# Kernel tuning notes

Measured on AMD Instinct MI355X. Metric: run time of the kernel, lower is better.

## Reference

```python
import jax, jax.numpy as jnp
import numpy as np

T_ITERS = 10
EPS = 1e-5


def setup_inputs() -> dict:
    key = jax.random.key(0)
    B, C, H, W = 64, 256, 56, 56
    X = jax.random.normal(key, (B, C, H, W), dtype=jnp.float32)
    # running_rot buffer: orthogonal rotation per group (g=1)
    M = np.random.default_rng(0).standard_normal((C, C)).astype(np.float32)
    q, _ = np.linalg.qr(M)
    running_rot = jnp.asarray(q[None, :, :])  # [g=1, d, d]
    return {"X": X, "running_rot": running_rot}


def _whiten(X, g, nc):
    # X: [B, C, H, W] -> x: [g, d, m] with m = B*H*W (training-mode IterNorm)
    B, C, H, W = X.shape
    x = jnp.transpose(X, (1, 0, 2, 3)).reshape(g, nc, -1)
    m = x.shape[-1]
    mean = jnp.mean(x, axis=-1, keepdims=True)          # [g, d, 1]
    xc = x - mean                                        # [g, d, m]
    I = jnp.broadcast_to(jnp.eye(nc, dtype=X.dtype), (g, nc, nc))
    Sigma = EPS * I + jnp.matmul(xc, jnp.swapaxes(xc, 1, 2)) * (1.0 / m)
    # rTr = 1 / trace(Sigma) per group
    rTr = 1.0 / jnp.sum(Sigma * I, axis=(1, 2), keepdims=True)  # [g,1,1]
    Sigma_N = Sigma * rTr
    # Newton-Schulz iteration: P_{k+1} = 1.5 P_k - 0.5 P_k^3 Sigma_N
    P = I
    for _ in range(T_ITERS):
        P3 = jnp.matmul(jnp.matmul(P, P), P)
        P = 1.5 * P - 0.5 * jnp.matmul(P3, Sigma_N)
    wm = P * jnp.sqrt(rTr)                               # whitening matrix [g,d,d]
    xn = jnp.matmul(wm, xc)                              # [g, d, m]
    return xn.reshape(C, B, H, W).transpose(1, 0, 2, 3)  # back to [B,C,H,W]


def reference(X, running_rot):
    g, _, nc = running_rot.shape
    B, C, H, W = X.shape
    X_hat = _whiten(X, g, nc)                            # [B, C, H, W]
    Xg = X_hat.reshape(B, g, nc, H, W)
    # rotate whitened features: Q^T alignment, einsum('bgchw,gdc->bgdhw')
    Xr = jnp.einsum('bgchw,gdc->bgdhw', Xg, running_rot)
    return Xr.reshape(B, C, H, W)
```

## Files before the change

kernel.cpp:

```cpp
#include <hip/hip_runtime.h>
#include <math.h>

#define HWn   3136
#define Cn    256
#define KCPB  49
#define NCHUNK 3136
#define INV_M (1.0f/200704.0f)
#define EPSc  1e-5f

typedef __attribute__((ext_vector_type(4))) float f32x4;
typedef __attribute__((ext_vector_type(8))) short s16x8;
typedef __attribute__((ext_vector_type(4))) unsigned short u16x4;

static __device__ __forceinline__ unsigned short f2bf(float f) {
  unsigned int u = __builtin_bit_cast(unsigned int, f);
  u = (u + 0x7fffu + ((u >> 16) & 1u)) >> 16;
  return (unsigned short)u;
}

__global__ __launch_bounds__(1024) void k_gram(const float* __restrict__ X,
                                               float* __restrict__ Gp,
                                               float* __restrict__ Sp,
                                               int nparts) {
  __shared__ __align__(16) unsigned short lds[2][256 * 64];
  const int t = threadIdx.x, p = blockIdx.x;
  const int w = t >> 6, l = t & 63, a = l & 15, g = l >> 4;
  const int swzA = (a & 7) << 3;
  const int crow = t >> 4, sg = t & 15;

  f32x4 acc[16];
#pragma unroll
  for (int j = 0; j < 16; ++j) acc[j] = (f32x4){0.f, 0.f, 0.f, 0.f};
  float sum4[4] = {0.f, 0.f, 0.f, 0.f};
  float vx[16];

  const int start = (int)(((long)NCHUNK * p) / nparts);
  const int end   = (int)(((long)NCHUNK * (p + 1)) / nparts);

#define G_LOADS(CH)                                                           \
  {                                                                           \
    const int b_ = (CH) / KCPB, kc_ = (CH) % KCPB;                            \
    const float* xb_ = X + (long)b_ * Cn * HWn + kc_ * 64;                    \
    _Pragma("unroll")                                                         \
    for (int p4 = 0; p4 < 4; ++p4) {                                          \
      const float4 v = *(const float4*)(xb_ + (long)(p4 * 64 + crow) * HWn + sg * 4); \
      vx[p4 * 4 + 0] = v.x; vx[p4 * 4 + 1] = v.y;                             \
      vx[p4 * 4 + 2] = v.z; vx[p4 * 4 + 3] = v.w;                             \
    }                                                                         \
  }

#define G_CVTWR(BUF)                                                          \
  {                                                                           \
    _Pragma("unroll")                                                         \
    for (int p4 = 0; p4 < 4; ++p4) {                                          \
      const int c_ = p4 * 64 + crow;                                          \
      sum4[p4] += (vx[p4 * 4 + 0] + vx[p4 * 4 + 1])                           \
                + (vx[p4 * 4 + 2] + vx[p4 * 4 + 3]);                          \
      u16x4 h;                                                                \
      h.x = f2bf(vx[p4 * 4 + 0]); h.y = f2bf(vx[p4 * 4 + 1]);                 \
      h.z = f2bf(vx[p4 * 4 + 2]); h.w = f2bf(vx[p4 * 4 + 3]);                 \
      *(u16x4*)(&lds[BUF][0] + ((c_ * 64 + sg * 4) ^ ((c_ & 7) << 3))) = h;   \
    }                                                                         \
  }

  G_LOADS(start);
  G_CVTWR(0);
  __syncthreads();

  for (int ch = start; ch < end; ++ch) {
    const int cur = (ch - start) & 1;
    if (ch + 1 < end) G_LOADS(ch + 1);
    const unsigned short* tile = &lds[cur][0];
#pragma unroll
    for (int kk = 0; kk < 64; kk += 32) {
      const s16x8 fw = *(const s16x8*)(tile + (((w * 16 + a) * 64 + kk + g * 8) ^ swzA));
#pragma unroll
      for (int j = 0; j < 16; ++j) {
        const s16x8 fj = *(const s16x8*)(tile + (((j * 16 + a) * 64 + kk + g * 8) ^ swzA));
        acc[j] = __builtin_amdgcn_mfma_f32_16x16x32_bf16(fw, fj, acc[j], 0, 0, 0);
      }
    }
    if (ch + 1 < end) G_CVTWR(cur ^ 1);
    __syncthreads();
  }
#undef G_LOADS
#undef G_CVTWR

  float* gout = Gp + (long)p * 65536;
#pragma unroll
  for (int j = 0; j < 16; ++j)
#pragma unroll
    for (int r = 0; r < 4; ++r)
      gout[(16 * w + 4 * g + r) * 256 + 16 * j + a] = acc[j][r];

#pragma unroll
  for (int p4 = 0; p4 < 4; ++p4) {
    float s = sum4[p4];
    s += __shfl_xor(s, 1);
    s += __shfl_xor(s, 2);
    s += __shfl_xor(s, 4);
    s += __shfl_xor(s, 8);
    if (a == 0) Sp[(long)p * 256 + p4 * 64 + w * 4 + g] = s;
  }
}

__global__ __launch_bounds__(1024) void k_reduce(const float* __restrict__ Gp,
                                                 const float* __restrict__ Sp,
                                                 float* __restrict__ Sigma,
                                                 float* __restrict__ P0,
                                                 float* __restrict__ diag,
                                                 float* __restrict__ meansum,
                                                 int nparts) {
  __shared__ float red[4][256];
  __shared__ float msh[256];
  const int t = threadIdx.x, c = t & 255, g = t >> 8, j = blockIdx.x;
  const long e = (long)j * 256 + c;
  const int p0 = (nparts * g) >> 2, p1 = (nparts * (g + 1)) >> 2;

  {
    float s = 0.f;
    for (int p = p0; p < p1; ++p) s += Sp[(long)p * 256 + c];
    red[g][c] = s;
  }
  __syncthreads();
  if (g == 0) msh[c] = (red[0][c] + red[1][c]) + (red[2][c] + red[3][c]);
  __syncthreads();

  {
    const float* gp = Gp + (long)p0 * 65536 + e;
    const int np = p1 - p0;
    float s0 = 0.f, s1 = 0.f, s2 = 0.f, s3 = 0.f;
    int p = 0;
#pragma unroll 2
    for (; p + 4 <= np; p += 4) {
      s0 += gp[(long)(p + 0) * 65536];
      s1 += gp[(long)(p + 1) * 65536];
      s2 += gp[(long)(p + 2) * 65536];
      s3 += gp[(long)(p + 3) * 65536];
    }
    for (; p < np; ++p) s0 += gp[(long)p * 65536];
    red[g][c] = (s0 + s1) + (s2 + s3);
  }
  __syncthreads();

  if (g == 0) {
    const float tot = (red[0][c] + red[1][c]) + (red[2][c] + red[3][c]);
    const float mc = msh[c] * INV_M;
    const float mj = msh[j] * INV_M;
    const float sig = tot * INV_M - mj * mc + ((j == c) ? EPSc : 0.f);
    Sigma[e] = sig;
    if (c == j) diag[j] = sig;
    if (j == 0) meansum[c] = msh[c];
  } else if (g == 1) {
    P0[e] = (j == c) ? 1.f : 0.f;
  }
}

__global__ void k_prep(const float* __restrict__ diag, float* __restrict__ scal) {
  __shared__ float r[256];
  const int c = threadIdx.x;
  r[c] = diag[c];
  __syncthreads();
  for (int st = 128; st > 0; st >>= 1) {
    if (c < st) r[c] += r[c + st];
    __syncthreads();
  }
  if (c == 0) {
    const float tr = r[0];
    scal[0] = tr;
    scal[1] = 1.0f / tr;
    scal[2] = sqrtf(1.0f / tr);
  }
}

__global__ __launch_bounds__(1024) void k_ns(const float* __restrict__ Ps,
                                             float* __restrict__ Pd,
                                             const float* __restrict__ Sig,
                                             const float* __restrict__ scal) {
  __shared__ __align__(16) float PT[256][4];
  __shared__ __align__(16) float red[4][256][4];
  const int t = threadIdx.x, c = t & 255, kh = t >> 8, k0 = kh * 64;
  const int r0 = blockIdx.x * 4;

  PT[c][kh] = Ps[(r0 + kh) * 256 + c];
  __syncthreads();

  f32x4 acc;

#define NS_PHASE(BPTR)                                                        \
  {                                                                           \
    acc = (f32x4){0.f, 0.f, 0.f, 0.f};                                        \
    const float* Bb = (BPTR) + (long)k0 * 256 + c;                            \
    _Pragma("unroll 8")                                                       \
    for (int kk = 0; kk < 64; ++kk) {                                         \
      const float b = Bb[(long)kk * 256];                                     \
      const f32x4 a4 = *(const f32x4*)&PT[k0 + kk][0];                        \
      acc += a4 * b;                                                          \
    }                                                                         \
    *(f32x4*)&red[kh][c][0] = acc;                                            \
    __syncthreads();                                                          \
  }

#define NS_COMBINE()                                                          \
  {                                                                           \
    const f32x4 vs = (*(const f32x4*)&red[0][c][0] + *(const f32x4*)&red[1][c][0]) \
                   + (*(const f32x4*)&red[2][c][0] + *(const f32x4*)&red[3][c][0]); \
    if (kh == 0) *(f32x4*)&PT[c][0] = vs;                                     \
    __syncthreads();                                                          \
  }

  NS_PHASE(Ps);
  NS_COMBINE();
  NS_PHASE(Ps);
  NS_COMBINE();
  NS_PHASE(Sig);

  const float rTr = scal[1];
  const float t3 = ((red[0][c][kh] + red[1][c][kh]) + (red[2][c][kh] + red[3][c][kh]));
  const float pr = Ps[(r0 + kh) * 256 + c];
  Pd[(r0 + kh) * 256 + c] = 1.5f * pr - 0.5f * rTr * t3;
#undef NS_PHASE
#undef NS_COMBINE
}

__global__ void k_makeA(const float* __restrict__ rot, const float* __restrict__ P,
                        const float* __restrict__ scal, const float* __restrict__ meansum,
                        unsigned short* __restrict__ Abf, float* __restrict__ bias) {
  __shared__ float Rw[8][256];
  __shared__ float Tw[8][256];
  const int r0 = blockIdx.x * 8, c = threadIdx.x;
#pragma unroll
  for (int r = 0; r < 8; ++r) Rw[r][c] = rot[(r0 + r) * 256 + c];
  __syncthreads();
  float t[8];
#pragma unroll
  for (int r = 0; r < 8; ++r) t[r] = 0.f;
  for (int k = 0; k < 256; ++k) {
    const float pv = P[k * 256 + c];
#pragma unroll
    for (int r = 0; r < 8; ++r) t[r] += Rw[r][k] * pv;
  }
  const float s = scal[2];
  const float mc = meansum[c] * INV_M;
#pragma unroll
  for (int r = 0; r < 8; ++r) {
    const float av = t[r] * s;
    Abf[(r0 + r) * 256 + c] = f2bf(av);
    Tw[r][c] = av * mc;
  }
  __syncthreads();
  for (int st = 128; st > 0; st >>= 1) {
    if (c < st) {
#pragma unroll
      for (int r = 0; r < 8; ++r) Tw[r][c] += Tw[r][c + st];
    }
    __syncthreads();
  }
  if (c == 0) {
#pragma unroll
    for (int r = 0; r < 8; ++r) bias[r0 + r] = Tw[r][0];
  }
}

__global__ __launch_bounds__(1024) void k_apply(const float* __restrict__ X,
                                                const unsigned short* __restrict__ Abf,
                                                const float* __restrict__ bias,
                                                float* __restrict__ out) {
  __shared__ __align__(16) unsigned short lds[2][64 * 256];
  const int t = threadIdx.x, w = t >> 6, l = t & 63, a = l & 15, g = l >> 4;
  const int bid = blockIdx.x;
  const int b = bid >> 3, strip = bid & 7;
  const int ch0 = (49 * strip) >> 3, ch1 = (49 * (strip + 1)) >> 3;

  const int d = 16 * w + a;
  s16x8 af[8];
#pragma unroll
  for (int kk8 = 0; kk8 < 8; ++kk8)
    af[kk8] = *(const s16x8*)(Abf + d * 256 + kk8 * 32 + g * 8);
  const float bd = bias[d];

  const float* xbase = X + (long)b * Cn * HWn;
  float* obase = out + (long)b * Cn * HWn;
  float vx[16];

#define A_LOADS(CH)                                                           \
  {                                                                           \
    const int s0_ = (CH) * 64;                                                \
    _Pragma("unroll")                                                         \
    for (int p4 = 0; p4 < 4; ++p4) {                                          \
      const int c4_ = p4 * 16 + w;                                            \
      const float* xp_ = xbase + (long)(c4_ * 4) * HWn + s0_ + l;             \
      vx[p4 * 4 + 0] = xp_[0];                                                \
      vx[p4 * 4 + 1] = xp_[HWn];                                              \
      vx[p4 * 4 + 2] = xp_[2 * HWn];                                          \
      vx[p4 * 4 + 3] = xp_[3 * HWn];                                          \
    }                                                                         \
  }

#define A_CVTWR(BUF)                                                          \
  {                                                                           \
    _Pragma("unroll")                                                         \
    for (int p4 = 0; p4 < 4; ++p4) {                                          \
      const int c4_ = p4 * 16 + w;                                            \
      u16x4 h;                                                                \
      h.x = f2bf(vx[p4 * 4 + 0]); h.y = f2bf(vx[p4 * 4 + 1]);                 \
      h.z = f2bf(vx[p4 * 4 + 2]); h.w = f2bf(vx[p4 * 4 + 3]);                 \
      *(u16x4*)(&lds[BUF][0] + ((l * 256 + c4_ * 4) ^ ((l & 7) << 3))) = h;   \
    }                                                                         \
  }

  A_LOADS(ch0);
  A_CVTWR(0);
  __syncthreads();

  for (int ch = ch0; ch < ch1; ++ch) {
    const int cur = (ch - ch0) & 1;
    if (ch + 1 < ch1) A_LOADS(ch + 1);

    const unsigned short* tile = &lds[cur][0];
    f32x4 acc[4];
#pragma unroll
    for (int st = 0; st < 4; ++st) acc[st] = (f32x4){0.f, 0.f, 0.f, 0.f};
#pragma unroll
    for (int kk8 = 0; kk8 < 8; ++kk8) {
#pragma unroll
      for (int st = 0; st < 4; ++st) {
        const s16x8 xf = *(const s16x8*)(tile + (((st * 16 + a) * 256 + kk8 * 32 + g * 8) ^ ((a & 7) << 3)));
        acc[st] = __builtin_amdgcn_mfma_f32_16x16x32_bf16(xf, af[kk8], acc[st], 0, 0, 0);
      }
    }
    const int s0 = ch * 64;
#pragma unroll
    for (int st = 0; st < 4; ++st) {
      const f32x4 o = acc[st] - bd;
      *(f32x4*)(obase + (long)d * HWn + s0 + st * 16 + 4 * g) = o;
    }

    if (ch + 1 < ch1) A_CVTWR(cur ^ 1);
    __syncthreads();
  }
#undef A_LOADS
#undef A_CVTWR
}

extern "C" void kernel_launch(void* const* d_in, const int* in_sizes, int n_in,
                              void* d_out, int out_size, void* d_ws, size_t ws_size,
                              hipStream_t stream) {
  const float* X = (const float*)d_in[0];
  const float* rot = (const float*)d_in[1];
  float* out = (float*)d_out;

  auto need = [](int np) -> size_t {
    return (size_t)4 * ((size_t)np * 65536 + (size_t)np * 256 + 3 * 65536
                        + 256 + 256 + 16 + 256)
         + (size_t)2 * 65536;
  };
  int nparts = 256;
  while (nparts > 4 && need(nparts) > ws_size) nparts >>= 1;

  float* w = (float*)d_ws;
  float* Gp = w;       w += (size_t)nparts * 65536;
  float* Sp = w;       w += (size_t)nparts * 256;
  float* Sigma = w;    w += 65536;
  float* P0 = w;       w += 65536;
  float* P1 = w;       w += 65536;
  float* diag = w;     w += 256;
  float* meansum = w;  w += 256;
  float* scal = w;     w += 16;
  float* bias = w;     w += 256;
  unsigned short* Abf = (unsigned short*)w;

  k_gram<<<dim3(nparts), dim3(1024), 0, stream>>>(X, Gp, Sp, nparts);
  k_reduce<<<dim3(256), dim3(1024), 0, stream>>>(Gp, Sp, Sigma, P0, diag, meansum, nparts);
  k_prep<<<dim3(1), dim3(256), 0, stream>>>(diag, scal);
  float* ps = P0;
  float* pd = P1;
  for (int i = 0; i < 10; ++i) {
    k_ns<<<dim3(64), dim3(1024), 0, stream>>>(ps, pd, Sigma, scal);
    float* tmp = ps; ps = pd; pd = tmp;
  }
  k_makeA<<<dim3(32), dim3(256), 0, stream>>>(rot, ps, scal, meansum, Abf, bias);
  k_apply<<<dim3(512), dim3(1024), 0, stream>>>(X, Abf, bias, out);
}
```

Measured before the change: 312.9 us.

## Peel first Newton-Schulz iteration, vectorize reduce, packed bf16 cvt, nontemporal stores

The first Newton-Schulz step with P=I is computed in closed form (1.5I - 0.5*Sigma_N) and fused with the trace reduction, which drops the identity init, k_prep, and one k_ns launch. k_reduce now sums the partial Grams with float4 loads split across 16 slices. Elsewhere the bf16 conversions use the packed hardware convert instruction, the output uses nontemporal stores, and nparts is halved to 128. The new convert rounding may differ slightly from the software rounding, and halving nparts shifts work between the gram and reduce kernels.

```diff
diff --git a/kernel.cpp b/kernel.cpp
--- a/kernel.cpp
+++ b/kernel.cpp
@@ -16,6 +16,12 @@
   unsigned int u = __builtin_bit_cast(unsigned int, f);
   u = (u + 0x7fffu + ((u >> 16) & 1u)) >> 16;
   return (unsigned short)u;
+}
+
+static __device__ __forceinline__ unsigned int cvt_pk_bf16(float lo, float hi) {
+  unsigned int r;
+  asm("v_cvt_pk_bf16_f32 %0, %1, %2" : "=v"(r) : "v"(lo), "v"(hi));
+  return r;
 }
 
 __global__ __launch_bounds__(1024) void k_gram(const float* __restrict__ X,
@@ -56,10 +62,10 @@
       const int c_ = p4 * 64 + crow;                                          \
       sum4[p4] += (vx[p4 * 4 + 0] + vx[p4 * 4 + 1])                           \
                 + (vx[p4 * 4 + 2] + vx[p4 * 4 + 3]);                          \
-      u16x4 h;                                                                \
-      h.x = f2bf(vx[p4 * 4 + 0]); h.y = f2bf(vx[p4 * 4 + 1]);                 \
-      h.z = f2bf(vx[p4 * 4 + 2]); h.w = f2bf(vx[p4 * 4 + 3]);                 \
-      *(u16x4*)(&lds[BUF][0] + ((c_ * 64 + sg * 4) ^ ((c_ & 7) << 3))) = h;   \
+      uint2 hh;                                                               \
+      hh.x = cvt_pk_bf16(vx[p4 * 4 + 0], vx[p4 * 4 + 1]);                     \
+      hh.y = cvt_pk_bf16(vx[p4 * 4 + 2], vx[p4 * 4 + 3]);                     \
+      *(uint2*)(&lds[BUF][0] + ((c_ * 64 + sg * 4) ^ ((c_ & 7) << 3))) = hh;  \
     }                                                                         \
   }
 
@@ -107,69 +113,68 @@
 __global__ __launch_bounds__(1024) void k_reduce(const float* __restrict__ Gp,
                                                  const float* __restrict__ Sp,
                                                  float* __restrict__ Sigma,
-                                                 float* __restrict__ P0,
                                                  float* __restrict__ diag,
                                                  float* __restrict__ meansum,
                                                  int nparts) {
-  __shared__ float red[4][256];
+  __shared__ float redA[4][256];
   __shared__ float msh[256];
-  const int t = threadIdx.x, c = t & 255, g = t >> 8, j = blockIdx.x;
-  const long e = (long)j * 256 + c;
-  const int p0 = (nparts * g) >> 2, p1 = (nparts * (g + 1)) >> 2;
+  __shared__ __align__(16) float redB[16][256];
+  const int t = threadIdx.x, j = blockIdx.x;
+  const int c = t & 255, g = t >> 8;
 
   {
     float s = 0.f;
-    for (int p = p0; p < p1; ++p) s += Sp[(long)p * 256 + c];
-    red[g][c] = s;
-  }
-  __syncthreads();
-  if (g == 0) msh[c] = (red[0][c] + red[1][c]) + (red[2][c] + red[3][c]);
-  __syncthreads();
+    const int pa0 = (nparts * g) >> 2, pa1 = (nparts * (g + 1)) >> 2;
+    for (int p = pa0; p < pa1; ++p) s += Sp[(long)p * 256 + c];
+    redA[g][c] = s;
+  }
+  __syncthreads();
+  if (g == 0) msh[c] = (redA[0][c] + redA[1][c]) + (redA[2][c] + redA[3][c]);
 
   {
-    const float* gp = Gp + (long)p0 * 65536 + e;
-    const int np = p1 - p0;
-    float s0 = 0.f, s1 = 0.f, s2 = 0.f, s3 = 0.f;
-    int p = 0;
-#pragma unroll 2
-    for (; p + 4 <= np; p += 4) {
-      s0 += gp[(long)(p + 0) * 65536];
-      s1 += gp[(long)(p + 1) * 65536];
-      s2 += gp[(long)(p + 2) * 65536];
-      s3 += gp[(long)(p + 3) * 65536];
-    }
-    for (; p < np; ++p) s0 += gp[(long)p * 65536];
-    red[g][c] = (s0 + s1) + (s2 + s3);
-  }
-  __syncthreads();
-
-  if (g == 0) {
-    const float tot = (red[0][c] + red[1][c]) + (red[2][c] + red[3][c]);
-    const float mc = msh[c] * INV_M;
+    const int c4 = (t & 63) * 4, sl = t >> 6;
+    const int pb0 = (nparts * sl) >> 4, pb1 = (nparts * (sl + 1)) >> 4;
+    const float* gp = Gp + (long)pb0 * 65536 + (long)j * 256 + c4;
+    f32x4 s4 = (f32x4){0.f, 0.f, 0.f, 0.f};
+    for (int p = pb0; p < pb1; ++p) { s4 += *(const f32x4*)gp; gp += 65536; }
+    *(f32x4*)&redB[sl][c4] = s4;
+  }
+  __syncthreads();
+
+  if (t < 256) {
+    float t0 = 0.f, t1 = 0.f;
+#pragma unroll
+    for (int sl = 0; sl < 16; sl += 2) { t0 += redB[sl][t]; t1 += redB[sl + 1][t]; }
+    const float tot = t0 + t1;
+    const float mc = msh[t] * INV_M;
     const float mj = msh[j] * INV_M;
-    const float sig = tot * INV_M - mj * mc + ((j == c) ? EPSc : 0.f);
-    Sigma[e] = sig;
-    if (c == j) diag[j] = sig;
-    if (j == 0) meansum[c] = msh[c];
-  } else if (g == 1) {
-    P0[e] = (j == c) ? 1.f : 0.f;
-  }
-}
-
-__global__ void k_prep(const float* __restrict__ diag, float* __restrict__ scal) {
-  __shared__ float r[256];
-  const int c = threadIdx.x;
-  r[c] = diag[c];
+    const float sig = tot * INV_M - mj * mc + ((j == t) ? EPSc : 0.f);
+    Sigma[(long)j * 256 + t] = sig;
+    if (t == j) diag[j] = sig;
+    if (j == 0) meansum[t] = msh[t];
+  }
+}
+
+__global__ __launch_bounds__(1024) void k_it0(const float* __restrict__ Sig,
+                                              const float* __restrict__ diag,
+                                              float* __restrict__ P1,
+                                              float* __restrict__ scal) {
+  __shared__ float trs[256];
+  const int t = threadIdx.x, c = t & 255, kh = t >> 8;
+  const int row = blockIdx.x * 4 + kh;
+  if (t < 256) trs[t] = diag[t];
   __syncthreads();
   for (int st = 128; st > 0; st >>= 1) {
-    if (c < st) r[c] += r[c + st];
+    if (t < st) trs[t] += trs[t + st];
     __syncthreads();
   }
-  if (c == 0) {
-    const float tr = r[0];
+  const float tr = trs[0];
+  const float rTr = 1.0f / tr;
+  P1[(long)row * 256 + c] = ((row == c) ? 1.5f : 0.f) - 0.5f * rTr * Sig[(long)row * 256 + c];
+  if (blockIdx.x == 0 && t == 0) {
     scal[0] = tr;
-    scal[1] = 1.0f / tr;
-    scal[2] = sqrtf(1.0f / tr);
+    scal[1] = rTr;
+    scal[2] = sqrtf(rTr);
   }
 }
 
@@ -302,10 +307,10 @@
     _Pragma("unroll")                                                         \
     for (int p4 = 0; p4 < 4; ++p4) {                                          \
       const int c4_ = p4 * 16 + w;                                            \
-      u16x4 h;                                                                \
-      h.x = f2bf(vx[p4 * 4 + 0]); h.y = f2bf(vx[p4 * 4 + 1]);                 \
-      h.z = f2bf(vx[p4 * 4 + 2]); h.w = f2bf(vx[p4 * 4 + 3]);                 \
-      *(u16x4*)(&lds[BUF][0] + ((l * 256 + c4_ * 4) ^ ((l & 7) << 3))) = h;   \
+      uint2 hh;                                                               \
+      hh.x = cvt_pk_bf16(vx[p4 * 4 + 0], vx[p4 * 4 + 1]);                     \
+      hh.y = cvt_pk_bf16(vx[p4 * 4 + 2], vx[p4 * 4 + 3]);                     \
+      *(uint2*)(&lds[BUF][0] + ((l * 256 + c4_ * 4) ^ ((l & 7) << 3))) = hh;  \
     }                                                                         \
   }
 
@@ -333,7 +338,7 @@
 #pragma unroll
     for (int st = 0; st < 4; ++st) {
       const f32x4 o = acc[st] - bd;
-      *(f32x4*)(obase + (long)d * HWn + s0 + st * 16 + 4 * g) = o;
+      __builtin_nontemporal_store(o, (f32x4*)(obase + (long)d * HWn + s0 + st * 16 + 4 * g));
     }
 
     if (ch + 1 < ch1) A_CVTWR(cur ^ 1);
@@ -355,7 +360,7 @@
                         + 256 + 256 + 16 + 256)
          + (size_t)2 * 65536;
   };
-  int nparts = 256;
+  int nparts = 128;
   while (nparts > 4 && need(nparts) > ws_size) nparts >>= 1;
 
   float* w = (float*)d_ws;
@@ -371,11 +376,11 @@
   unsigned short* Abf = (unsigned short*)w;
 
   k_gram<<<dim3(nparts), dim3(1024), 0, stream>>>(X, Gp, Sp, nparts);
-  k_reduce<<<dim3(256), dim3(1024), 0, stream>>>(Gp, Sp, Sigma, P0, diag, meansum, nparts);
-  k_prep<<<dim3(1), dim3(256), 0, stream>>>(diag, scal);
-  float* ps = P0;
-  float* pd = P1;
-  for (int i = 0; i < 10; ++i) {
+  k_reduce<<<dim3(256), dim3(1024), 0, stream>>>(Gp, Sp, Sigma, diag, meansum, nparts);
+  k_it0<<<dim3(64), dim3(1024), 0, stream>>>(Sigma, diag, P1, scal);
+  float* ps = P1;
+  float* pd = P0;
+  for (int i = 0; i < 9; ++i) {
     k_ns<<<dim3(64), dim3(1024), 0, stream>>>(ps, pd, Sigma, scal);
     float* tmp = ps; ps = pd; pd = tmp;
   }
```

New measurement: 297.6 us. 1.05x faster.
